# Kernel optimization log

Hardware: AMD Instinct MI355X
Metric: run time of the kernel (lower is better)

Reference implementation:

```python
import jax, jax.numpy as jnp
import numpy as np

BATCH, N_SEQS, SEQ_LEN, D_IN, D_OUT = 8, 4, 2048, 512, 512
LN_EPS = 1e-5


def setup_inputs() -> dict:
    key = jax.random.key(0)
    ks = jax.random.split(key, 6)
    s_in = 1.0 / np.sqrt(D_IN)
    s_out = 1.0 / np.sqrt(D_OUT)
    return {
        "x": jax.random.normal(ks[0], (BATCH, N_SEQS * SEQ_LEN * D_IN), dtype=jnp.float32),
        "Wq": jax.random.normal(ks[1], (D_OUT, D_IN), dtype=jnp.float32) * s_in,
        "Wk": jax.random.normal(ks[2], (D_OUT, D_IN), dtype=jnp.float32) * s_in,
        "Wv": jax.random.normal(ks[3], (D_OUT, D_IN), dtype=jnp.float32) * s_in,
        "Wo": jax.random.normal(ks[4], (D_OUT, D_OUT), dtype=jnp.float32) * s_out,
        "bo": jnp.zeros((D_OUT,), dtype=jnp.float32),
        "gamma": jnp.ones((D_OUT,), dtype=jnp.float32),
        "beta": jnp.zeros((D_OUT,), dtype=jnp.float32),
    }


def _phi(x):
    # positive feature map: elu(x) + 1
    return jax.nn.elu(x) + 1.0


def reference(x, Wq, Wk, Wv, Wo, bo, gamma, beta):
    batch = x.shape[0]
    xs = x.reshape(batch * N_SEQS, SEQ_LEN, D_IN)  # [B*L, S, d_in]
    Q = _phi(jnp.einsum('bsi,oi->bso', xs, Wq))     # [B*L, S, d_out]
    K = _phi(jnp.einsum('bsi,oi->bso', xs, Wk))
    V = jnp.einsum('bsi,oi->bso', xs, Wv)
    kv = jnp.einsum('bsd,bse->bde', K, V)           # [B*L, d_out, d_out]
    num = jnp.einsum('bsd,bde->bse', Q, kv)         # [B*L, S, d_out]
    k_sum = K.sum(axis=1, keepdims=True)            # [B*L, 1, d_out]
    den = jnp.maximum((Q * k_sum).sum(axis=-1, keepdims=True), 1e-6)
    out = num / den
    y = jnp.einsum('bse,oe->bso', out, Wo) + bo + out  # out_proj + residual
    mu = y.mean(axis=-1, keepdims=True)
    var = ((y - mu) ** 2).mean(axis=-1, keepdims=True)
    y = (y - mu) * jax.lax.rsqrt(var + LN_EPS) * gamma + beta
    return y.reshape(batch, -1)
```

## Files before the change

### kernel.cpp

```cpp
#include <hip/hip_runtime.h>
#include <cstdint>

typedef __bf16 bf16x8 __attribute__((ext_vector_type(8)));
typedef float  f32x4  __attribute__((ext_vector_type(4)));

#define SEQS   32
#define SLEN   2048
#define DIM    512
#define MROWS  65536

static __device__ __forceinline__ void load_lds16(const void* g, void* l) {
  __builtin_amdgcn_global_load_lds(
      (const __attribute__((address_space(1))) void*)(uintptr_t)g,
      (__attribute__((address_space(3))) void*)(uintptr_t)l,
      16, 0, 0);
}

static __device__ __forceinline__ unsigned short bfbits(float f) {
  __bf16 h = (__bf16)f;
  unsigned short u;
  __builtin_memcpy(&u, &h, 2);
  return u;
}

static __device__ __forceinline__ void gemm_core(
    const __bf16* __restrict__ A, int lda, int arow0,
    const __bf16* __restrict__ B, int ldb, int brow0,
    int K, __bf16* Asm, __bf16* Bsm, f32x4 (&acc)[4][4])
{
  const int tid  = threadIdx.x;
  const int wave = tid >> 6;
  const int lane = tid & 63;
  const int wr = wave >> 1, wc = wave & 1;
  const int lr = lane & 15, kq = lane >> 4;

  for (int kt = 0; kt < K; kt += 64) {
#pragma unroll
    for (int q = 0; q < 4; ++q) {
      const int L  = q * 4096 + tid * 16;
      const int r  = L >> 7;
      const int sl = (L >> 4) & 7;
      const int c  = ((sl ^ (r & 7)) << 3);
      load_lds16(A + (size_t)(arow0 + r) * lda + (kt + c),
                 (char*)Asm + q * 4096 + wave * 1024);
      load_lds16(B + (size_t)(brow0 + r) * ldb + (kt + c),
                 (char*)Bsm + q * 4096 + wave * 1024);
    }
    __syncthreads();

    bf16x8 af[2][4], bfr[2][4];
#pragma unroll
    for (int kk = 0; kk < 2; ++kk)
#pragma unroll
      for (int i = 0; i < 4; ++i) {
        const int rA = wr * 64 + i * 16 + lr;
        af[kk][i] = *reinterpret_cast<const bf16x8*>(
            (char*)Asm + rA * 128 + ((((kk * 4 + kq) ^ (rA & 7))) << 4));
        const int rB = wc * 64 + i * 16 + lr;
        bfr[kk][i] = *reinterpret_cast<const bf16x8*>(
            (char*)Bsm + rB * 128 + ((((kk * 4 + kq) ^ (rB & 7))) << 4));
      }
#pragma unroll
    for (int kk = 0; kk < 2; ++kk)
#pragma unroll
      for (int i = 0; i < 4; ++i)
#pragma unroll
        for (int j = 0; j < 4; ++j)
          acc[i][j] = __builtin_amdgcn_mfma_f32_16x16x32_bf16(
              af[kk][i], bfr[kk][j], acc[i][j], 0, 0, 0);
    __syncthreads();
  }
}


__global__ __launch_bounds__(256) void cast_kernel(
    const float* __restrict__ src, __bf16* __restrict__ dst, int n8)
{
  int i = blockIdx.x * blockDim.x + threadIdx.x;
  const int stride = gridDim.x * blockDim.x;
  for (; i < n8; i += stride) {
    const float4* p = reinterpret_cast<const float4*>(src + (size_t)i * 8);
    float4 a = p[0], b2 = p[1];
    float vals[8] = {a.x, a.y, a.z, a.w, b2.x, b2.y, b2.z, b2.w};
    uint32_t w[4];
#pragma unroll
    for (int t = 0; t < 4; ++t)
      w[t] = (uint32_t)bfbits(vals[2 * t]) | ((uint32_t)bfbits(vals[2 * t + 1]) << 16);
    uint4 o; o.x = w[0]; o.y = w[1]; o.z = w[2]; o.w = w[3];
    *reinterpret_cast<uint4*>(dst + (size_t)i * 8) = o;
  }
}

__global__ __launch_bounds__(256) void cast4_kernel(
    const float* __restrict__ a, const float* __restrict__ b,
    const float* __restrict__ c, const float* __restrict__ d,
    __bf16* __restrict__ ab, __bf16* __restrict__ bb,
    __bf16* __restrict__ cb, __bf16* __restrict__ db)
{
  const int z = blockIdx.y;
  const float* src = (z == 0) ? a : (z == 1) ? b : (z == 2) ? c : d;
  __bf16* dst = (z == 0) ? ab : (z == 1) ? bb : (z == 2) ? cb : db;
  const int i = blockIdx.x * 256 + threadIdx.x;
  const float4* p = reinterpret_cast<const float4*>(src + (size_t)i * 8);
  float4 x = p[0], y = p[1];
  float vals[8] = {x.x, x.y, x.z, x.w, y.x, y.y, y.z, y.w};
  uint32_t w[4];
#pragma unroll
  for (int t = 0; t < 4; ++t)
    w[t] = (uint32_t)bfbits(vals[2 * t]) | ((uint32_t)bfbits(vals[2 * t + 1]) << 16);
  uint4 o; o.x = w[0]; o.y = w[1]; o.z = w[2]; o.w = w[3];
  *reinterpret_cast<uint4*>(dst + (size_t)i * 8) = o;
}

__global__ __launch_bounds__(512, 1) void qkv_kernel(
    const __bf16* __restrict__ xb,
    const __bf16* __restrict__ Wqb, const __bf16* __restrict__ Wkb,
    const __bf16* __restrict__ Wvb,
    __bf16* __restrict__ Q, __bf16* __restrict__ KT, __bf16* __restrict__ VT,
    float* __restrict__ ksum)
{
  __shared__ __align__(16) __bf16 As[2][256 * 32];
  __shared__ __align__(16) __bf16 Bs[2][256 * 32];
  const int b = blockIdx.x;
  const int xcd = b & 7, loc = b >> 3;
  const int brow = (loc / 6) * 8 + xcd;
  const int inner = loc % 6;
  const int z = inner >> 1, bcol = inner & 1;
  const __bf16* W = (z == 0) ? Wqb : (z == 1) ? Wkb : Wvb;

  const int tid = threadIdx.x, wave = tid >> 6, lane = tid & 63;
  const int wr = wave >> 2, wn = wave & 3;
  const int lr = lane & 15, kq = lane >> 4;

  const __bf16* Abase = xb + (size_t)(brow * 256) * DIM;
  const __bf16* Bbase = W + (size_t)(bcol * 256) * DIM;

  auto stage = [&](int s, int kt) {
#pragma unroll
    for (int q = 0; q < 2; ++q) {
      const int L  = q * 8192 + tid * 16;
      const int r  = L >> 6;
      const int sl = (L >> 4) & 3;
      const int c  = ((sl ^ ((r >> 1) & 3)) << 3);
      load_lds16(Abase + (size_t)r * DIM + (kt + c),
                 (char*)As[s] + q * 8192 + wave * 1024);
      load_lds16(Bbase + (size_t)r * DIM + (kt + c),
                 (char*)Bs[s] + q * 8192 + wave * 1024);
    }
  };

  f32x4 acc[8][4] = {};
  stage(0, 0);
  __syncthreads();
  for (int t = 0; t < 16; ++t) {
    const int cur = t & 1;
    if (t < 15) stage(cur ^ 1, (t + 1) * 32);
    const char* Ac = (const char*)As[cur];
    const char* Bc = (const char*)Bs[cur];
    bf16x8 bfr[4], af[8];
#pragma unroll
    for (int j = 0; j < 4; ++j) {
      const int rB = wn * 64 + j * 16 + lr;
      bfr[j] = *reinterpret_cast<const bf16x8*>(
          Bc + rB * 64 + ((kq ^ ((rB >> 1) & 3)) << 4));
    }
#pragma unroll
    for (int i = 0; i < 8; ++i) {
      const int rA = wr * 128 + i * 16 + lr;
      af[i] = *reinterpret_cast<const bf16x8*>(
          Ac + rA * 64 + ((kq ^ ((rA >> 1) & 3)) << 4));
    }
#pragma unroll
    for (int i = 0; i < 8; ++i)
#pragma unroll
      for (int j = 0; j < 4; ++j)
        acc[i][j] = __builtin_amdgcn_mfma_f32_16x16x32_bf16(af[i], bfr[j], acc[i][j], 0, 0, 0);
    __syncthreads();
  }

  const int m00 = brow * 256 + wr * 128 + kq * 4;
  const int n00 = bcol * 256 + wn * 64 + lr;
  if (z == 0) {
#pragma unroll
    for (int i = 0; i < 8; ++i)
#pragma unroll
      for (int j = 0; j < 4; ++j) {
        const int n = n00 + j * 16;
#pragma unroll
        for (int r = 0; r < 4; ++r) {
          const int m = m00 + i * 16 + r;
          float v = acc[i][j][r];
          v = (v > 0.f) ? (v + 1.f) : __expf(v);
          Q[(size_t)m * DIM + n] = (__bf16)v;
        }
      }
  } else {
    __bf16* T = (z == 1) ? KT : VT;
    const int seq = (brow * 256) >> 11;
    float ks[4] = {0.f, 0.f, 0.f, 0.f};
#pragma unroll
    for (int i = 0; i < 8; ++i) {
      const int mb = m00 + i * 16;
      const int s0 = mb & 2047;
#pragma unroll
      for (int j = 0; j < 4; ++j) {
        const int d = n00 + j * 16;
        unsigned short h[4];
#pragma unroll
        for (int r = 0; r < 4; ++r) {
          float v = acc[i][j][r];
          if (z == 1) { v = (v > 0.f) ? (v + 1.f) : __expf(v); ks[j] += v; }
          h[r] = bfbits(v);
        }
        uint2 u;
        u.x = (uint32_t)h[0] | ((uint32_t)h[1] << 16);
        u.y = (uint32_t)h[2] | ((uint32_t)h[3] << 16);
        *reinterpret_cast<uint2*>(T + ((size_t)(seq * DIM + d) << 11) + s0) = u;
      }
    }
    if (z == 1) {
#pragma unroll
      for (int j = 0; j < 4; ++j) {
        float p = ks[j];
        p += __shfl_xor(p, 16, 64);
        p += __shfl_xor(p, 32, 64);
        if (kq == 0) atomicAdd(&ksum[seq * DIM + n00 + j * 16], p);
      }
    }
  }
}

__global__ __launch_bounds__(256) void den_kernel(
    const __bf16* __restrict__ Q, const float* __restrict__ ksum,
    float* __restrict__ den)
{
  const int lane = threadIdx.x & 63;
  const int m = blockIdx.x * 4 + (threadIdx.x >> 6);
  bf16x8 qv = *reinterpret_cast<const bf16x8*>(Q + (size_t)m * DIM + lane * 8);
  const float* kp = ksum + ((m >> 11) << 9) + lane * 8;
  float s = 0.f;
#pragma unroll
  for (int t = 0; t < 8; ++t) s += (float)qv[t] * kp[t];
#pragma unroll
  for (int off = 32; off > 0; off >>= 1) s += __shfl_xor(s, off, 64);
  if (lane == 0) den[m] = fmaxf(s, 1e-6f);
}

__global__ __launch_bounds__(256) void kv_kernel(
    const __bf16* __restrict__ VT, const __bf16* __restrict__ KT,
    __bf16* __restrict__ kvT)
{
  __shared__ __align__(16) __bf16 Asm[128 * 64];
  __shared__ __align__(16) __bf16 Bsm[128 * 64];
  const int b = blockIdx.x;
  const int xcd = b & 7, loc = b >> 3;
  const int seq = (loc >> 4) * 8 + xcd;
  const int inner = loc & 15;
  const int bxx = inner >> 2, byy = inner & 3;
  const __bf16* A = VT + (size_t)seq * DIM * SLEN;
  const __bf16* B = KT + (size_t)seq * DIM * SLEN;
  f32x4 acc[4][4] = {};
  gemm_core(A, SLEN, bxx * 128, B, SLEN, byy * 128, SLEN, Asm, Bsm, acc);

  const int tid = threadIdx.x, wave = tid >> 6, lane = tid & 63;
  const int wr = wave >> 1, wc = wave & 1, lr = lane & 15, kq = lane >> 4;
  const int m0 = bxx * 128 + wr * 64 + kq * 4;
  const int n0 = byy * 128 + wc * 64 + lr;
  __bf16* C = kvT + (size_t)seq * DIM * DIM;
#pragma unroll
  for (int i = 0; i < 4; ++i)
#pragma unroll
    for (int j = 0; j < 4; ++j)
#pragma unroll
      for (int r = 0; r < 4; ++r)
        C[(size_t)(m0 + i * 16 + r) * DIM + (n0 + j * 16)] = (__bf16)acc[i][j][r];
}

__global__ __launch_bounds__(256) void num_kernel(
    const __bf16* __restrict__ Q, const __bf16* __restrict__ kvT,
    const float* __restrict__ den, __bf16* __restrict__ out)
{
  __shared__ __align__(16) __bf16 Asm[128 * 64];
  __shared__ __align__(16) __bf16 Bsm[128 * 64];
  const int b = blockIdx.x;
  const int xcd = b & 7, loc = b >> 3;
  const int seq = (loc >> 6) * 8 + xcd;
  const int inner = loc & 63;
  const int brow = seq * 16 + (inner >> 2);
  const int bcol = inner & 3;
  f32x4 acc[4][4] = {};
  gemm_core(Q, DIM, brow * 128, kvT + (size_t)seq * DIM * DIM, DIM,
            bcol * 128, DIM, Asm, Bsm, acc);

  const int tid = threadIdx.x, wave = tid >> 6, lane = tid & 63;
  const int wr = wave >> 1, wc = wave & 1, lr = lane & 15, kq = lane >> 4;
  const int m0 = brow * 128 + wr * 64 + kq * 4;
  const int n0 = bcol * 128 + wc * 64 + lr;
  float rden[4][4];
#pragma unroll
  for (int i = 0; i < 4; ++i)
#pragma unroll
    for (int r = 0; r < 4; ++r)
      rden[i][r] = 1.f / den[m0 + i * 16 + r];
#pragma unroll
  for (int i = 0; i < 4; ++i)
#pragma unroll
    for (int j = 0; j < 4; ++j)
#pragma unroll
      for (int r = 0; r < 4; ++r)
        out[(size_t)(m0 + i * 16 + r) * DIM + (n0 + j * 16)] =
            (__bf16)(acc[i][j][r] * rden[i][r]);
}

__global__ __launch_bounds__(512, 1) void final_kernel(
    const __bf16* __restrict__ outb, const __bf16* __restrict__ Wob,
    const float* __restrict__ bo, const float* __restrict__ gamma,
    const float* __restrict__ beta, float* __restrict__ y)
{
  __shared__ __align__(16) __bf16 Asm[128 * 32];
  __shared__ __align__(16) __bf16 Bsm[512 * 32];
  __shared__ float redS[2][128], redSS[2][128];
  const int tid = threadIdx.x, wave = tid >> 6, lane = tid & 63;
  const int Wr = wave >> 1, Wc = wave & 1;
  const int lr = lane & 15, kq = lane >> 4;
  const int brow = blockIdx.x;
  f32x4 acc[2][16] = {};

  for (int kt = 0; kt < DIM; kt += 32) {
    {
      const int L = tid * 16;
      const int r = L >> 6, sl = (L >> 4) & 3;
      const int c = ((sl ^ ((r >> 1) & 3)) << 3);
      load_lds16(outb + (size_t)(brow * 128 + r) * DIM + (kt + c),
                 (char*)Asm + wave * 1024);
    }
#pragma unroll
    for (int q = 0; q < 4; ++q) {
      const int L = q * 8192 + tid * 16;
      const int r = L >> 6, sl = (L >> 4) & 3;
      const int c = ((sl ^ ((r >> 1) & 3)) << 3);
      load_lds16(Wob + (size_t)r * DIM + (kt + c),
                 (char*)Bsm + q * 8192 + wave * 1024);
    }
    __syncthreads();
    bf16x8 af[2];
#pragma unroll
    for (int i = 0; i < 2; ++i) {
      const int rA = Wr * 32 + i * 16 + lr;
      af[i] = *reinterpret_cast<const bf16x8*>(
          (char*)Asm + rA * 64 + ((kq ^ ((rA >> 1) & 3)) << 4));
    }
#pragma unroll
    for (int j = 0; j < 16; ++j) {
      const int rB = Wc * 256 + j * 16 + lr;
      bf16x8 bf = *reinterpret_cast<const bf16x8*>(
          (char*)Bsm + rB * 64 + ((kq ^ ((rB >> 1) & 3)) << 4));
#pragma unroll
      for (int i = 0; i < 2; ++i)
        acc[i][j] = __builtin_amdgcn_mfma_f32_16x16x32_bf16(af[i], bf, acc[i][j], 0, 0, 0);
    }
    __syncthreads();
  }

  const int m0g = brow * 128;
  float sA[2][4] = {{0.f}}, ssA[2][4] = {{0.f}};
#pragma unroll
  for (int j = 0; j < 16; ++j) {
    const int n = Wc * 256 + j * 16 + lr;
    const float bon = bo[n];
#pragma unroll
    for (int i = 0; i < 2; ++i) {
      const int mb = m0g + Wr * 32 + i * 16 + kq * 4;
#pragma unroll
      for (int r = 0; r < 4; ++r) {
        float v = acc[i][j][r] + bon + (float)outb[(size_t)(mb + r) * DIM + n];
        acc[i][j][r] = v;
        sA[i][r] += v; ssA[i][r] += v * v;
      }
    }
  }
#pragma unroll
  for (int i = 0; i < 2; ++i)
#pragma unroll
    for (int r = 0; r < 4; ++r) {
      float s = sA[i][r], ss = ssA[i][r];
#pragma unroll
      for (int off = 1; off <= 8; off <<= 1) {
        s  += __shfl_xor(s,  off, 64);
        ss += __shfl_xor(ss, off, 64);
      }
      if (lr == 0) {
        const int ml = Wr * 32 + i * 16 + kq * 4 + r;
        redS[Wc][ml] = s; redSS[Wc][ml] = ss;
      }
    }
  __syncthreads();
  float mu_[2][4], rs_[2][4];
#pragma unroll
  for (int i = 0; i < 2; ++i)
#pragma unroll
    for (int r = 0; r < 4; ++r) {
      const int ml = Wr * 32 + i * 16 + kq * 4 + r;
      const float S  = redS[0][ml]  + redS[1][ml];
      const float SS = redSS[0][ml] + redSS[1][ml];
      const float mu = S * (1.f / 512.f);
      const float var = SS * (1.f / 512.f) - mu * mu;
      mu_[i][r] = mu;
      rs_[i][r] = rsqrtf(var + 1e-5f);
    }
#pragma unroll
  for (int j = 0; j < 16; ++j) {
    const int n = Wc * 256 + j * 16 + lr;
    const float g = gamma[n], bb = beta[n];
#pragma unroll
    for (int i = 0; i < 2; ++i) {
      const int mb = m0g + Wr * 32 + i * 16 + kq * 4;
#pragma unroll
      for (int r = 0; r < 4; ++r)
        y[(size_t)(mb + r) * DIM + n] = (acc[i][j][r] - mu_[i][r]) * rs_[i][r] * g + bb;
    }
  }
}

extern "C" void kernel_launch(void* const* d_in, const int* in_sizes, int n_in,
                              void* d_out, int out_size, void* d_ws, size_t ws_size,
                              hipStream_t stream)
{
  const float* x     = (const float*)d_in[0];
  const float* Wq    = (const float*)d_in[1];
  const float* Wk    = (const float*)d_in[2];
  const float* Wv    = (const float*)d_in[3];
  const float* Wo    = (const float*)d_in[4];
  const float* bo    = (const float*)d_in[5];
  const float* gamma = (const float*)d_in[6];
  const float* beta  = (const float*)d_in[7];
  float* outp = (float*)d_out;

  char* ws = (char*)d_ws;
  const size_t SZ = 67108864;
  __bf16* xb   = (__bf16*)(ws + 0);
  __bf16* Q    = (__bf16*)(ws + SZ);
  __bf16* KT   = (__bf16*)(ws + 2 * SZ);
  __bf16* VT   = (__bf16*)(ws + 3 * SZ);
  __bf16* kvT  = (__bf16*)(ws + 4 * SZ);
  __bf16* Wqb  = (__bf16*)(ws + 4 * SZ + 16777216);
  __bf16* Wkb  = Wqb + 262144;
  __bf16* Wvb  = Wkb + 262144;
  __bf16* Wob  = Wvb + 262144;
  float*  ksum = (float*)(Wob + 262144);
  float*  den  = (float*)((char*)ksum + 65536);

  hipMemsetAsync(ksum, 0, SEQS * DIM * sizeof(float), stream);
  cast_kernel<<<4096, 256, 0, stream>>>(x, xb, MROWS * DIM / 8);
  cast4_kernel<<<dim3(128, 4), 256, 0, stream>>>(Wq, Wk, Wv, Wo, Wqb, Wkb, Wvb, Wob);

  qkv_kernel<<<1536, 512, 0, stream>>>(xb, Wqb, Wkb, Wvb, Q, KT, VT, ksum);
  den_kernel<<<16384, 256, 0, stream>>>(Q, ksum, den);
  kv_kernel<<<512, 256, 0, stream>>>(VT, KT, kvT);
  num_kernel<<<2048, 256, 0, stream>>>(Q, kvT, den, xb );
  final_kernel<<<512, 512, 0, stream>>>(xb, Wob, bo, gamma, beta, outp);
}
```

Measured before the change: 421.0 us.

## Fuse fp32-to-bf16 cast of x into QKV GEMM A-tile loading

Removes the standalone cast kernel for x. The QKV GEMM now reads fp32 x directly into registers, converts it to bf16 and writes it into the swizzled LDS tile after the MFMA block, which overlaps the next tile's global loads with compute. This drops one full write and read of a 64 MB bf16 copy of x. In exchange, each QKV block reads twice the bytes for A, and because every row tile is reused by 6 column/projection blocks, x is converted redundantly. A also now goes through a register path instead of direct-to-LDS loads, adding register pressure.

```diff
diff --git a/kernel.cpp b/kernel.cpp
--- a/kernel.cpp
+++ b/kernel.cpp
@@ -73,24 +73,6 @@
 }
 
 
-__global__ __launch_bounds__(256) void cast_kernel(
-    const float* __restrict__ src, __bf16* __restrict__ dst, int n8)
-{
-  int i = blockIdx.x * blockDim.x + threadIdx.x;
-  const int stride = gridDim.x * blockDim.x;
-  for (; i < n8; i += stride) {
-    const float4* p = reinterpret_cast<const float4*>(src + (size_t)i * 8);
-    float4 a = p[0], b2 = p[1];
-    float vals[8] = {a.x, a.y, a.z, a.w, b2.x, b2.y, b2.z, b2.w};
-    uint32_t w[4];
-#pragma unroll
-    for (int t = 0; t < 4; ++t)
-      w[t] = (uint32_t)bfbits(vals[2 * t]) | ((uint32_t)bfbits(vals[2 * t + 1]) << 16);
-    uint4 o; o.x = w[0]; o.y = w[1]; o.z = w[2]; o.w = w[3];
-    *reinterpret_cast<uint4*>(dst + (size_t)i * 8) = o;
-  }
-}
-
 __global__ __launch_bounds__(256) void cast4_kernel(
     const float* __restrict__ a, const float* __restrict__ b,
     const float* __restrict__ c, const float* __restrict__ d,
@@ -113,7 +95,7 @@
 }
 
 __global__ __launch_bounds__(512, 1) void qkv_kernel(
-    const __bf16* __restrict__ xb,
+    const float* __restrict__ x,
     const __bf16* __restrict__ Wqb, const __bf16* __restrict__ Wkb,
     const __bf16* __restrict__ Wvb,
     __bf16* __restrict__ Q, __bf16* __restrict__ KT, __bf16* __restrict__ VT,
@@ -132,49 +114,76 @@
   const int wr = wave >> 2, wn = wave & 3;
   const int lr = lane & 15, kq = lane >> 4;
 
-  const __bf16* Abase = xb + (size_t)(brow * 256) * DIM;
+  const float*  Abase = x + (size_t)(brow * 256) * DIM;
   const __bf16* Bbase = W + (size_t)(bcol * 256) * DIM;
 
-  auto stage = [&](int s, int kt) {
-#pragma unroll
-    for (int q = 0; q < 2; ++q) {
-      const int L  = q * 8192 + tid * 16;
-      const int r  = L >> 6;
-      const int sl = (L >> 4) & 3;
+  const int arow_t = tid >> 3;
+  const int acol_t = (tid & 7) * 4;
+  const int a_sl = (tid & 7) >> 1, a_h = (tid & 1) * 8;
+
+  float4 ga[4];
+  auto issue_gA = [&](int kt) {
+#pragma unroll
+    for (int p = 0; p < 4; ++p) {
+      const int r = p * 64 + arow_t;
+      ga[p] = *reinterpret_cast<const float4*>(Abase + (size_t)r * DIM + kt + acol_t);
+    }
+  };
+  auto write_A = [&](int s) {
+#pragma unroll
+    for (int p = 0; p < 4; ++p) {
+      const int r = p * 64 + arow_t;
+      uint2 u;
+      u.x = (uint32_t)bfbits(ga[p].x) | ((uint32_t)bfbits(ga[p].y) << 16);
+      u.y = (uint32_t)bfbits(ga[p].z) | ((uint32_t)bfbits(ga[p].w) << 16);
+      const int byte = r * 64 + ((a_sl ^ ((r >> 1) & 3)) << 4) + a_h;
+      *reinterpret_cast<uint2*>((char*)(&As[s][0]) + byte) = u;
+    }
+  };
+  auto stage_B = [&](int s, int kt) {
+#pragma unroll
+    for (int p = 0; p < 2; ++p) {
+      const int r  = p * 128 + (tid >> 2);
+      const int sl = tid & 3;
       const int c  = ((sl ^ ((r >> 1) & 3)) << 3);
-      load_lds16(Abase + (size_t)r * DIM + (kt + c),
-                 (char*)As[s] + q * 8192 + wave * 1024);
       load_lds16(Bbase + (size_t)r * DIM + (kt + c),
-                 (char*)Bs[s] + q * 8192 + wave * 1024);
+                 (char*)(&Bs[s][0]) + p * 8192 + wave * 1024);
     }
   };
 
   f32x4 acc[8][4] = {};
-  stage(0, 0);
+
+  issue_gA(0);
+  stage_B(0, 0);
+  write_A(0);
   __syncthreads();
+
   for (int t = 0; t < 16; ++t) {
     const int cur = t & 1;
-    if (t < 15) stage(cur ^ 1, (t + 1) * 32);
-    const char* Ac = (const char*)As[cur];
-    const char* Bc = (const char*)Bs[cur];
+    if (t < 15) {
+      issue_gA((t + 1) * 32);
+      stage_B(cur ^ 1, (t + 1) * 32);
+    }
     bf16x8 bfr[4], af[8];
 #pragma unroll
     for (int j = 0; j < 4; ++j) {
       const int rB = wn * 64 + j * 16 + lr;
       bfr[j] = *reinterpret_cast<const bf16x8*>(
-          Bc + rB * 64 + ((kq ^ ((rB >> 1) & 3)) << 4));
+          (const char*)(&Bs[cur][0]) + rB * 64 + ((kq ^ ((rB >> 1) & 3)) << 4));
     }
 #pragma unroll
     for (int i = 0; i < 8; ++i) {
       const int rA = wr * 128 + i * 16 + lr;
       af[i] = *reinterpret_cast<const bf16x8*>(
-          Ac + rA * 64 + ((kq ^ ((rA >> 1) & 3)) << 4));
+          (const char*)(&As[cur][0]) + rA * 64 + ((kq ^ ((rA >> 1) & 3)) << 4));
     }
 #pragma unroll
     for (int i = 0; i < 8; ++i)
 #pragma unroll
       for (int j = 0; j < 4; ++j)
         acc[i][j] = __builtin_amdgcn_mfma_f32_16x16x32_bf16(af[i], bfr[j], acc[i][j], 0, 0, 0);
+
+    if (t < 15) write_A(cur ^ 1);
     __syncthreads();
   }
 
@@ -438,7 +447,7 @@
 
   char* ws = (char*)d_ws;
   const size_t SZ = 67108864;
-  __bf16* xb   = (__bf16*)(ws + 0);
+  __bf16* outB = (__bf16*)(ws + 0);
   __bf16* Q    = (__bf16*)(ws + SZ);
   __bf16* KT   = (__bf16*)(ws + 2 * SZ);
   __bf16* VT   = (__bf16*)(ws + 3 * SZ);
@@ -451,12 +460,11 @@
   float*  den  = (float*)((char*)ksum + 65536);
 
   hipMemsetAsync(ksum, 0, SEQS * DIM * sizeof(float), stream);
-  cast_kernel<<<4096, 256, 0, stream>>>(x, xb, MROWS * DIM / 8);
   cast4_kernel<<<dim3(128, 4), 256, 0, stream>>>(Wq, Wk, Wv, Wo, Wqb, Wkb, Wvb, Wob);
 
-  qkv_kernel<<<1536, 512, 0, stream>>>(xb, Wqb, Wkb, Wvb, Q, KT, VT, ksum);
+  qkv_kernel<<<1536, 512, 0, stream>>>(x, Wqb, Wkb, Wvb, Q, KT, VT, ksum);
   den_kernel<<<16384, 256, 0, stream>>>(Q, ksum, den);
   kv_kernel<<<512, 256, 0, stream>>>(VT, KT, kvT);
-  num_kernel<<<2048, 256, 0, stream>>>(Q, kvT, den, xb );
-  final_kernel<<<512, 512, 0, stream>>>(xb, Wob, bo, gamma, beta, outp);
-}
+  num_kernel<<<2048, 256, 0, stream>>>(Q, kvT, den, outB);
+  final_kernel<<<512, 512, 0, stream>>>(outB, Wob, bo, gamma, beta, outp);
+}
```

After: 480.5 us. +14.1%, slower.

## Deepen QKV K-tile to 64 and double-buffer final out-proj GEMM

Applied to the files above, without the earlier changes.

In the QKV GEMM, each K step now loads 64 columns instead of 32, with a new 128-byte-row XOR swizzle. That halves the number of barrier-separated iterations. In the final out-projection+LayerNorm kernel, LDS is double-buffered so the next tile's global-to-LDS loads overlap the MFMAs on the current tile, where before it was load, sync, compute, sync. LDS use grows from 64KB to 128KB in the QKV kernel and doubles in the final kernel, which could limit occupancy or exceed LDS limits.

```diff
diff --git a/kernel.cpp b/kernel.cpp
--- a/kernel.cpp
+++ b/kernel.cpp
@@ -119,8 +119,8 @@
     __bf16* __restrict__ Q, __bf16* __restrict__ KT, __bf16* __restrict__ VT,
     float* __restrict__ ksum)
 {
-  __shared__ __align__(16) __bf16 As[2][256 * 32];
-  __shared__ __align__(16) __bf16 Bs[2][256 * 32];
+  __shared__ __align__(16) __bf16 As[2][256 * 64];
+  __shared__ __align__(16) __bf16 Bs[2][256 * 64];
   const int b = blockIdx.x;
   const int xcd = b & 7, loc = b >> 3;
   const int brow = (loc / 6) * 8 + xcd;
@@ -137,44 +137,46 @@
 
   auto stage = [&](int s, int kt) {
 #pragma unroll
-    for (int q = 0; q < 2; ++q) {
+    for (int q = 0; q < 4; ++q) {
       const int L  = q * 8192 + tid * 16;
-      const int r  = L >> 6;
-      const int sl = (L >> 4) & 3;
-      const int c  = ((sl ^ ((r >> 1) & 3)) << 3);
+      const int r  = L >> 7;
+      const int sl = (L >> 4) & 7;
+      const int c  = ((sl ^ (r & 7)) << 3);
       load_lds16(Abase + (size_t)r * DIM + (kt + c),
-                 (char*)As[s] + q * 8192 + wave * 1024);
+                 (char*)(&As[s][0]) + q * 8192 + wave * 1024);
       load_lds16(Bbase + (size_t)r * DIM + (kt + c),
-                 (char*)Bs[s] + q * 8192 + wave * 1024);
+                 (char*)(&Bs[s][0]) + q * 8192 + wave * 1024);
     }
   };
 
   f32x4 acc[8][4] = {};
+
   stage(0, 0);
   __syncthreads();
-  for (int t = 0; t < 16; ++t) {
+  for (int t = 0; t < 8; ++t) {
     const int cur = t & 1;
-    if (t < 15) stage(cur ^ 1, (t + 1) * 32);
-    const char* Ac = (const char*)As[cur];
-    const char* Bc = (const char*)Bs[cur];
-    bf16x8 bfr[4], af[8];
-#pragma unroll
-    for (int j = 0; j < 4; ++j) {
-      const int rB = wn * 64 + j * 16 + lr;
-      bfr[j] = *reinterpret_cast<const bf16x8*>(
-          Bc + rB * 64 + ((kq ^ ((rB >> 1) & 3)) << 4));
-    }
-#pragma unroll
-    for (int i = 0; i < 8; ++i) {
-      const int rA = wr * 128 + i * 16 + lr;
-      af[i] = *reinterpret_cast<const bf16x8*>(
-          Ac + rA * 64 + ((kq ^ ((rA >> 1) & 3)) << 4));
-    }
-#pragma unroll
-    for (int i = 0; i < 8; ++i)
-#pragma unroll
-      for (int j = 0; j < 4; ++j)
-        acc[i][j] = __builtin_amdgcn_mfma_f32_16x16x32_bf16(af[i], bfr[j], acc[i][j], 0, 0, 0);
+    if (t < 7) stage(cur ^ 1, (t + 1) * 64);
+#pragma unroll
+    for (int kk = 0; kk < 2; ++kk) {
+      bf16x8 bfr[4], af[8];
+#pragma unroll
+      for (int j = 0; j < 4; ++j) {
+        const int rB = wn * 64 + j * 16 + lr;
+        bfr[j] = *reinterpret_cast<const bf16x8*>(
+            (const char*)(&Bs[cur][0]) + rB * 128 + (((kk * 4 + kq) ^ (rB & 7)) << 4));
+      }
+#pragma unroll
+      for (int i = 0; i < 8; ++i) {
+        const int rA = wr * 128 + i * 16 + lr;
+        af[i] = *reinterpret_cast<const bf16x8*>(
+            (const char*)(&As[cur][0]) + rA * 128 + (((kk * 4 + kq) ^ (rA & 7)) << 4));
+      }
+#pragma unroll
+      for (int i = 0; i < 8; ++i)
+#pragma unroll
+        for (int j = 0; j < 4; ++j)
+          acc[i][j] = __builtin_amdgcn_mfma_f32_16x16x32_bf16(af[i], bfr[j], acc[i][j], 0, 0, 0);
+    }
     __syncthreads();
   }
 
@@ -317,8 +319,8 @@
     const float* __restrict__ bo, const float* __restrict__ gamma,
     const float* __restrict__ beta, float* __restrict__ y)
 {
-  __shared__ __align__(16) __bf16 Asm[128 * 32];
-  __shared__ __align__(16) __bf16 Bsm[512 * 32];
+  __shared__ __align__(16) __bf16 Asm[2][128 * 32];
+  __shared__ __align__(16) __bf16 Bsm[2][512 * 32];
   __shared__ float redS[2][128], redSS[2][128];
   const int tid = threadIdx.x, wave = tid >> 6, lane = tid & 63;
   const int Wr = wave >> 1, Wc = wave & 1;
@@ -326,13 +328,13 @@
   const int brow = blockIdx.x;
   f32x4 acc[2][16] = {};
 
-  for (int kt = 0; kt < DIM; kt += 32) {
+  auto stage = [&](int s, int kt) {
     {
       const int L = tid * 16;
       const int r = L >> 6, sl = (L >> 4) & 3;
       const int c = ((sl ^ ((r >> 1) & 3)) << 3);
       load_lds16(outb + (size_t)(brow * 128 + r) * DIM + (kt + c),
-                 (char*)Asm + wave * 1024);
+                 (char*)(&Asm[s][0]) + wave * 1024);
     }
 #pragma unroll
     for (int q = 0; q < 4; ++q) {
@@ -340,21 +342,27 @@
       const int r = L >> 6, sl = (L >> 4) & 3;
       const int c = ((sl ^ ((r >> 1) & 3)) << 3);
       load_lds16(Wob + (size_t)r * DIM + (kt + c),
-                 (char*)Bsm + q * 8192 + wave * 1024);
-    }
-    __syncthreads();
+                 (char*)(&Bsm[s][0]) + q * 8192 + wave * 1024);
+    }
+  };
+
+  stage(0, 0);
+  __syncthreads();
+  for (int t = 0; t < 16; ++t) {
+    const int cur = t & 1;
+    if (t < 15) stage(cur ^ 1, (t + 1) * 32);
     bf16x8 af[2];
 #pragma unroll
     for (int i = 0; i < 2; ++i) {
       const int rA = Wr * 32 + i * 16 + lr;
       af[i] = *reinterpret_cast<const bf16x8*>(
-          (char*)Asm + rA * 64 + ((kq ^ ((rA >> 1) & 3)) << 4));
+          (char*)(&Asm[cur][0]) + rA * 64 + ((kq ^ ((rA >> 1) & 3)) << 4));
     }
 #pragma unroll
     for (int j = 0; j < 16; ++j) {
       const int rB = Wc * 256 + j * 16 + lr;
       bf16x8 bf = *reinterpret_cast<const bf16x8*>(
-          (char*)Bsm + rB * 64 + ((kq ^ ((rB >> 1) & 3)) << 4));
+          (char*)(&Bsm[cur][0]) + rB * 64 + ((kq ^ ((rB >> 1) & 3)) << 4));
 #pragma unroll
       for (int i = 0; i < 2; ++i)
         acc[i][j] = __builtin_amdgcn_mfma_f32_16x16x32_bf16(af[i], bf, acc[i][j], 0, 0, 0);
```

Result: faster. 398.9 us (-5.2%).
